# Kernel optimization log

Measured on AMD Instinct MI355X. Metric: run time of the kernel, lower is better.

## Reference

```python
import jax, jax.numpy as jnp
import numpy as np

IS, OS, H = 168, 24, 256           # input window, output horizon, state_hsize
TAU, MAXIMUM = 0.1, 1.0            # tau parameter (non-grad) and series maximum
DILS = [[1, 4], [16, 64]]          # ResidualDRNN groups of dilations


def _lstm(x, wih, whh, bih, bhh):
    """Single-layer LSTM over time-major x: (T, B, C). PyTorch gate order i,f,g,o."""
    def step(carry, xt):
        h, c = carry
        g = xt @ wih.T + h @ whh.T + (bih + bhh)
        i, f, gg, o = jnp.split(g, 4, axis=-1)
        c = jax.nn.sigmoid(f) * c + jax.nn.sigmoid(i) * jnp.tanh(gg)
        h = jax.nn.sigmoid(o) * jnp.tanh(c)
        return (h, c), h
    h0 = jnp.zeros((x.shape[1], H), x.dtype)
    _, hs = jax.lax.scan(step, (h0, h0), x)
    return hs


def _dilated_lstm(x, d, p):
    """Standard DRNN layer: pad T to multiple of d, interleave time into batch, run LSTM."""
    T, B, C = x.shape
    n = -(-T // d)
    xp = jnp.pad(x, ((0, n * d - T), (0, 0), (0, 0)))
    hd = _lstm(xp.reshape(n, d * B, C), *p)
    return hd.reshape(n * d, B, H)[:T]


def _forward(train, init_lev_sm, lstm_params, nl_w, nl_b, sc_w, sc_b):
    B, T = train.shape
    a = jax.nn.sigmoid(init_lev_sm[0])            # lev_sms (idxs are all 0 -> same scalar)
    floor = TAU * MAXIMUM                          # tau * maximum
    # --- exponential-smoothing level recurrence (sequential) ---
    lev0 = jnp.maximum(train[:, 0], floor)
    def step(lev, xt):
        new = jnp.maximum(a * xt + (1.0 - a) * lev, floor)
        return new, new
    _, rest = jax.lax.scan(step, lev0, train[:, 1:].T)
    levs = jnp.concatenate([lev0[None], rest], axis=0).T   # [B, T]
    # --- windowed normalization ---
    w_idx = jnp.arange(IS - 1, T)                           # W = T - IS + 1 window ends
    in_win = train[:, (w_idx - IS + 1)[:, None] + jnp.arange(IS)[None, :]]
    in_win = (in_win / levs[:, w_idx][:, :, None]).transpose(1, 0, 2)    # [W, B, IS]
    o_idx = jnp.arange(IS - 1, T - OS)                      # W_out = T - OS - IS + 1
    out_win = train[:, (o_idx + 1)[:, None] + jnp.arange(OS)[None, :]]
    out_win = (out_win / levs[:, o_idx][:, :, None]).transpose(1, 0, 2)  # [W_out, B, OS]
    # --- ResidualDRNN stack on window_input[:-OS] (time-major: windows are the sequence) ---
    x = in_win[:-OS]
    li = 0
    for g, dils in enumerate(DILS):
        residual = x
        h = x
        for d in dils:
            h = _dilated_lstm(h, d, lstm_params[li])
            li += 1
        x = h + residual if g > 0 else h                    # dropout p=0 -> identity
    x = jnp.tanh(x @ nl_w.T + nl_b)                         # add_nl_layer
    pred = x @ sc_w.T + sc_b                                # scoring
    return pred, out_win


def setup_inputs() -> dict:
    key = jax.random.key(0)
    ks = list(jax.random.split(key, 32))
    B, T = 32, 1024
    inp = {
        "train": jax.random.uniform(ks[0], (B, T), jnp.float32, 0.05, 1.0),
        "val": jax.random.uniform(ks[1], (B, T), jnp.float32, 0.05, 1.0),
        "test": jax.random.uniform(ks[2], (B, T), jnp.float32, 0.05, 1.0),
        "idxs": jnp.zeros((B,), jnp.int32),
        "init_lev_sm": jnp.array([0.5], jnp.float32),
    }
    sizes = [IS, H, H, H]  # input feature size of each of the 4 DRNN layers
    k = 3
    s = 1.0 / np.sqrt(H)
    for i, cin in enumerate(sizes):
        inp[f"wih{i}"] = jax.random.uniform(ks[k], (4 * H, cin), jnp.float32, -s, s); k += 1
        inp[f"whh{i}"] = jax.random.uniform(ks[k], (4 * H, H), jnp.float32, -s, s); k += 1
        inp[f"bih{i}"] = jax.random.uniform(ks[k], (4 * H,), jnp.float32, -s, s); k += 1
        inp[f"bhh{i}"] = jax.random.uniform(ks[k], (4 * H,), jnp.float32, -s, s); k += 1
    inp["nl_w"] = jax.random.uniform(ks[k], (H, H), jnp.float32, -s, s); k += 1
    inp["nl_b"] = jnp.zeros((H,), jnp.float32)
    inp["sc_w"] = jax.random.uniform(ks[k], (OS, H), jnp.float32, -s, s); k += 1
    inp["sc_b"] = jnp.zeros((OS,), jnp.float32)
    return inp


def reference(train, val, test, idxs, init_lev_sm,
              wih0, whh0, bih0, bhh0, wih1, whh1, bih1, bhh1,
              wih2, whh2, bih2, bhh2, wih3, whh3, bih3, bhh3,
              nl_w, nl_b, sc_w, sc_b):
    lstm_params = [(wih0, whh0, bih0, bhh0), (wih1, whh1, bih1, bhh1),
                   (wih2, whh2, bih2, bhh2), (wih3, whh3, bih3, bhh3)]
    # training path (validating=False, testing=False): only `train` is used
    return _forward(train, init_lev_sm, lstm_params, nl_w, nl_b, sc_w, sc_b)
```

## Files before the change

kernel.cpp:

```cpp
#include <hip/hip_runtime.h>
#include <hip/hip_fp16.h>
#include <math.h>

#define TT 833
#define GDIM 1024

typedef _Float16 f16x8 __attribute__((ext_vector_type(8)));
typedef float    f32x4 __attribute__((ext_vector_type(4)));

#if __has_builtin(__builtin_amdgcn_rcpf)
__device__ __forceinline__ float frcp(float x){ return __builtin_amdgcn_rcpf(x); }
#else
__device__ __forceinline__ float frcp(float x){ return 1.f/x; }
#endif

#if __has_builtin(__builtin_amdgcn_sdot4)
__device__ __forceinline__ int sdot4(unsigned a, unsigned b, int c){
  return __builtin_amdgcn_sdot4((int)a, (int)b, c, false);
}
#else
__device__ __forceinline__ int sdot4(unsigned a, unsigned b, int c){
  int ai = (int)a, bi = (int)b;
  c += ((ai<<24)>>24)*((bi<<24)>>24);
  c += ((ai<<16)>>24)*((bi<<16)>>24);
  c += ((ai<<8)>>24)*((bi<<8)>>24);
  c += (ai>>24)*(bi>>24);
  return c;
}
#endif


__global__ void levels_k(const float* __restrict__ train, const float* __restrict__ ism,
                         float* __restrict__ levs){
  int b = threadIdx.x;
  if (b >= 32) return;
  float a = 1.f/(1.f+expf(-ism[0]));
  const float* tr = train + b*1024;
  float* lv = levs + b*1024;
  float lev = fmaxf(tr[0], 0.1f);
  lv[0] = lev;
  for (int t = 1; t < 1024; ++t){
    lev = fmaxf(a*tr[t] + (1.f-a)*lev, 0.1f);
    lv[t] = lev;
  }
}

__global__ void win_x_k(const float* __restrict__ train, const float* __restrict__ levs,
                        float* __restrict__ x0){
  int idx = blockIdx.x*256 + threadIdx.x;
  int i = idx % 168;
  int r = idx / 168;
  int b = r & 31;
  int t = r >> 5;
  x0[idx] = train[b*1024 + t + i] / levs[b*1024 + t + 167];
}

__global__ void win_out_k(const float* __restrict__ train, const float* __restrict__ levs,
                          float* __restrict__ ow){
  int idx = blockIdx.x*256 + threadIdx.x;
  int o = idx % 24;
  int r = idx / 24;
  int b = r & 31;
  int t = r >> 5;
  ow[idx] = train[b*1024 + 168 + t + o] / levs[b*1024 + t + 167];
}

__global__ void permw_k(const float* __restrict__ wih, const float* __restrict__ bih,
                        const float* __restrict__ bhh, float* __restrict__ wP,
                        float* __restrict__ bP, int K){
  int t = blockIdx.x;
  int g = ((t & 3) << 8) + (t >> 2);
  for (int k = threadIdx.x; k < K; k += 256)
    wP[(size_t)t*K + k] = wih[(size_t)g*K + k];
  if (threadIdx.x == 0) bP[t] = bih[g] + bhh[g];
}

__global__ void packq_k(const float* __restrict__ w, uint4* __restrict__ wq,
                        float* __restrict__ sc){
  int t = blockIdx.x*256 + threadIdx.x;
  if (t >= 1024) return;
  int g = ((t & 3) << 8) + (t >> 2);
  const float* row = w + (size_t)g*256;
  float amax = 0.f;
  for (int k = 0; k < 256; ++k) amax = fmaxf(amax, fabsf(row[k]));
  amax = fmaxf(amax, 1e-20f);
  float s = amax/127.f, inv = 127.f/amax;
  sc[t] = s;
  for (int k16 = 0; k16 < 16; ++k16){
    union { uint4 u; signed char b[16]; } r;
    #pragma unroll
    for (int j = 0; j < 16; ++j){
      float q = rintf(row[k16*16 + j]*inv);
      q = fminf(fmaxf(q, -127.f), 127.f);
      r.b[j] = (signed char)q;
    }
    wq[(size_t)k16*1024 + t] = r.u;
  }
}

__global__ __launch_bounds__(256) void proj_mfma(
    const float* __restrict__ A, const float* __restrict__ W,
    const float* __restrict__ b1, const float* __restrict__ b2,
    float* __restrict__ C, int Mout, int K, int N, int dil, int act, int outHalf)
{
  __shared__ _Float16 As[128*40];
  __shared__ _Float16 Bs[128*40];
  const int tid = threadIdx.x;
  const int lane = tid & 63;
  const int w = tid >> 6, wr = w >> 1, wc = w & 1;
  const int m0 = blockIdx.y << 7, n0 = blockIdx.x << 7;

  const int rowA = tid >> 1;
  int srcrow;
  {
    int m = m0 + rowA;
    if (dil == 0) srcrow = (m < Mout) ? m : -1;
    else {
      int rows = dil << 5;
      int j = m / rows;
      int q = m - j*rows;
      int t = j*dil + (q >> 5);
      srcrow = (t < TT) ? ((t << 5) + (q & 31)) : -1;
    }
  }
  const int halfsel = tid & 1;
  const int nrow = n0 + rowA;

  f32x4 acc[4][4];
  #pragma unroll
  for (int i = 0; i < 4; ++i)
    #pragma unroll
    for (int j = 0; j < 4; ++j) acc[i][j] = (f32x4){0.f,0.f,0.f,0.f};

  const int nkt = (K + 31) >> 5;
  for (int kt = 0; kt < nkt; ++kt){
    const int k0 = (kt << 5) + halfsel*16;
    {
      union { uint4 u[2]; _Float16 h[16]; } tmp;
      if (srcrow >= 0 && k0 + 16 <= K){
        const float* s = A + (size_t)srcrow*K + k0;
        #pragma unroll
        for (int j = 0; j < 4; ++j){
          float4 v = *reinterpret_cast<const float4*>(s + j*4);
          tmp.h[j*4+0]=(_Float16)v.x; tmp.h[j*4+1]=(_Float16)v.y;
          tmp.h[j*4+2]=(_Float16)v.z; tmp.h[j*4+3]=(_Float16)v.w;
        }
      } else {
        const float* s = (srcrow >= 0) ? A + (size_t)srcrow*K : nullptr;
        #pragma unroll
        for (int j = 0; j < 16; ++j){
          int kk = k0 + j;
          tmp.h[j] = (s && kk < K) ? (_Float16)s[kk] : (_Float16)0.f;
        }
      }
      uint4* dst = reinterpret_cast<uint4*>(&As[rowA*40 + halfsel*16]);
      dst[0] = tmp.u[0]; dst[1] = tmp.u[1];
    }
    {
      union { uint4 u[2]; _Float16 h[16]; } tmp;
      if (k0 + 16 <= K){
        const float* s = W + (size_t)nrow*K + k0;
        #pragma unroll
        for (int j = 0; j < 4; ++j){
          float4 v = *reinterpret_cast<const float4*>(s + j*4);
          tmp.h[j*4+0]=(_Float16)v.x; tmp.h[j*4+1]=(_Float16)v.y;
          tmp.h[j*4+2]=(_Float16)v.z; tmp.h[j*4+3]=(_Float16)v.w;
        }
      } else {
        const float* s = W + (size_t)nrow*K;
        #pragma unroll
        for (int j = 0; j < 16; ++j){
          int kk = k0 + j;
          tmp.h[j] = (kk < K) ? (_Float16)s[kk] : (_Float16)0.f;
        }
      }
      uint4* dst = reinterpret_cast<uint4*>(&Bs[rowA*40 + halfsel*16]);
      dst[0] = tmp.u[0]; dst[1] = tmp.u[1];
    }
    __syncthreads();
    {
      const int kg = lane >> 4, r16 = lane & 15;
      f16x8 af[4], bf[4];
      #pragma unroll
      for (int mi = 0; mi < 4; ++mi)
        af[mi] = *reinterpret_cast<const f16x8*>(&As[(wr*64 + mi*16 + r16)*40 + kg*8]);
      #pragma unroll
      for (int nj = 0; nj < 4; ++nj)
        bf[nj] = *reinterpret_cast<const f16x8*>(&Bs[(wc*64 + nj*16 + r16)*40 + kg*8]);
      #pragma unroll
      for (int mi = 0; mi < 4; ++mi)
        #pragma unroll
        for (int nj = 0; nj < 4; ++nj)
          acc[mi][nj] = __builtin_amdgcn_mfma_f32_16x16x32_f16(af[mi], bf[nj], acc[mi][nj], 0, 0, 0);
    }
    __syncthreads();
  }
  #pragma unroll
  for (int mi = 0; mi < 4; ++mi){
    #pragma unroll
    for (int p = 0; p < 4; ++p){
      int mrow = m0 + wr*64 + mi*16 + (lane >> 4)*4 + p;
      if (mrow >= Mout) continue;
      #pragma unroll
      for (int nj = 0; nj < 4; ++nj){
        int ncol = n0 + wc*64 + nj*16 + (lane & 15);
        float v = acc[mi][nj][p] + b1[ncol] + (b2 ? b2[ncol] : 0.f);
        if (act) v = tanhf(v);
        if (outHalf) reinterpret_cast<__half*>(C)[(size_t)mrow*N + ncol] = __float2half(v);
        else C[(size_t)mrow*N + ncol] = v;
      }
    }
  }
}

template<int NR>
__global__ __launch_bounds__(512, 1) void srecr2_k(
    const uint4* __restrict__ wq, const float* __restrict__ scale,
    const __half* __restrict__ Gin,
    float* __restrict__ out, const float* __restrict__ res,
    int nsteps, int d, int rowsTotal)
{
  __shared__ __align__(16) unsigned int hq[2][NR][64];
  const int tid = threadIdx.x;
  const int s = tid & 1;
  const int j = tid >> 1;
  const int q0 = blockIdx.x*NR;
  const float sg0 = scale[2*tid]*(1.f/127.f);
  const float sg1 = scale[2*tid + 1]*(1.f/127.f);
  uint4 w0_[16], w1_[16];
  #pragma unroll
  for (int kk = 0; kk < 16; ++kk){
    w0_[kk] = wq[(size_t)kk*1024 + 2*tid];
    w1_[kk] = wq[(size_t)kk*1024 + 2*tid + 1];
  }
  float c[NR];
  #pragma unroll
  for (int rr = 0; rr < NR; ++rr) c[rr] = 0.f;
  for (int e = tid; e < 2*NR*64; e += 512) (&hq[0][0][0])[e] = 0u;
  __syncthreads();

  for (int step = 0; step < nsteps; ++step){
    const int cur = step & 1;
    const __half2* gbase = reinterpret_cast<const __half2*>(
        Gin + ((size_t)step*rowsTotal + q0)*GDIM);
    #pragma unroll
    for (int rr = 0; rr < NR; ++rr){
      __half2 g2 = gbase[rr*512 + tid];
      float gin0 = __half2float(__low2half(g2));
      float gin1 = __half2float(__high2half(g2));
      int a00 = 0, a01 = 0, a10 = 0, a11 = 0;
      #pragma unroll
      for (int k16 = 0; k16 < 8; ++k16){
        uint4 ha = *reinterpret_cast<const uint4*>(&hq[cur][rr][4*k16]);
        a00 = sdot4(w0_[k16].x, ha.x, a00); a00 = sdot4(w0_[k16].y, ha.y, a00);
        a00 = sdot4(w0_[k16].z, ha.z, a00); a00 = sdot4(w0_[k16].w, ha.w, a00);
        a10 = sdot4(w1_[k16].x, ha.x, a10); a10 = sdot4(w1_[k16].y, ha.y, a10);
        a10 = sdot4(w1_[k16].z, ha.z, a10); a10 = sdot4(w1_[k16].w, ha.w, a10);
        uint4 hb = *reinterpret_cast<const uint4*>(&hq[cur][rr][4*(k16 + 8)]);
        a01 = sdot4(w0_[k16+8].x, hb.x, a01); a01 = sdot4(w0_[k16+8].y, hb.y, a01);
        a01 = sdot4(w0_[k16+8].z, hb.z, a01); a01 = sdot4(w0_[k16+8].w, hb.w, a01);
        a11 = sdot4(w1_[k16+8].x, hb.x, a11); a11 = sdot4(w1_[k16+8].y, hb.y, a11);
        a11 = sdot4(w1_[k16+8].z, hb.z, a11); a11 = sdot4(w1_[k16+8].w, hb.w, a11);
      }
      float p0 = fmaf((float)(a00 + a01), sg0, gin0);
      float p1 = fmaf((float)(a10 + a11), sg1, gin1);
      float px0 = s ? p0 + p0 : p0;
      float t0 = frcp(1.f + __expf(-px0));
      float a0v = s ? fmaf(2.f, t0, -1.f) : t0;
      float a1v = frcp(1.f + __expf(-p1));
      float b0 = __shfl_xor(a0v, 1);
      float b1 = __shfl_xor(a1v, 1);
      float iv = s ? b0 : a0v;
      float fv = s ? b1 : a1v;
      float gv = s ? a0v : b0;
      float ov = s ? a1v : b1;
      float cn = fmaf(fv, c[rr], iv*gv);
      c[rr] = cn;
      if (s == 0){
        float e2 = __expf(-2.f*cn);
        float h = ov*(1.f - e2)*frcp(1.f + e2);
        int qh = (int)rintf(h*127.f);
        reinterpret_cast<signed char*>(&hq[cur^1][rr][0])[j] = (signed char)qh;
        int q = q0 + rr;
        int tg = step*d + (q >> 5);
        if (tg < TT){
          size_t oi = ((size_t)tg*32 + (q & 31))*256 + j;
          out[oi] = res ? (h + res[oi]) : h;
        }
      }
    }
    __syncthreads();
  }
}

template<int NR>
__global__ __launch_bounds__(1024) void srecq_k(
    const uint4* __restrict__ wq, const float* __restrict__ scale,
    const __half* __restrict__ Gin,
    float* __restrict__ out, const float* __restrict__ res,
    int nsteps, int d, int rowsTotal)
{
  __shared__ __align__(16) unsigned int hq[2][NR][64];
  const int tid = threadIdx.x;
  const int lane = tid & 63;
  const int base = lane & ~3;
  const int kg = tid & 3;
  const int j = tid >> 2;
  const int q0 = blockIdx.x*NR;
  const float sg = scale[tid]*(1.f/127.f);
  float c[NR];
  #pragma unroll
  for (int rr = 0; rr < NR; ++rr) c[rr] = 0.f;
  for (int e = tid; e < 2*NR*64; e += 1024) (&hq[0][0][0])[e] = 0u;
  __syncthreads();

  for (int step = 0; step < nsteps; ++step){
    const int cur = step & 1;
    float gin[NR];
    const __half* gbase = Gin + ((size_t)step*rowsTotal + q0)*GDIM;
    #pragma unroll
    for (int rr = 0; rr < NR; ++rr) gin[rr] = __half2float(gbase[rr*GDIM + tid]);
    int acc[NR];
    #pragma unroll
    for (int rr = 0; rr < NR; ++rr) acc[rr] = 0;
    #pragma unroll 4
    for (int k16 = 0; k16 < 16; ++k16){
      uint4 w = wq[(size_t)k16*1024 + tid];
      #pragma unroll
      for (int rr = 0; rr < NR; ++rr){
        uint4 h4 = *reinterpret_cast<const uint4*>(&hq[cur][rr][4*k16]);
        acc[rr] = sdot4(w.x, h4.x, acc[rr]);
        acc[rr] = sdot4(w.y, h4.y, acc[rr]);
        acc[rr] = sdot4(w.z, h4.z, acc[rr]);
        acc[rr] = sdot4(w.w, h4.w, acc[rr]);
      }
    }
    #pragma unroll
    for (int rr = 0; rr < NR; ++rr){
      float p = fmaf((float)acc[rr], sg, gin[rr]);
      float px = (kg == 2) ? p + p : p;
      float s = frcp(1.f + __expf(-px));
      float a = (kg == 2) ? fmaf(2.f, s, -1.f) : s;
      float iv = __shfl(a, base + 0);
      float fv = __shfl(a, base + 1);
      float gv = __shfl(a, base + 2);
      float ov = __shfl(a, base + 3);
      float cn = fmaf(fv, c[rr], iv*gv);
      c[rr] = cn;
      float e2 = __expf(-2.f*cn);
      float h = ov*(1.f - e2)*frcp(1.f + e2);
      if (kg == 0){
        int qh = (int)rintf(h*127.f);
        reinterpret_cast<signed char*>(&hq[cur^1][rr][0])[j] = (signed char)qh;
        int q = q0 + rr;
        int tg = step*d + (q >> 5);
        if (tg < TT){
          size_t oi = ((size_t)tg*32 + (q & 31))*256 + j;
          out[oi] = res ? (h + res[oi]) : h;
        }
      }
    }
    __syncthreads();
  }
}

__global__ __launch_bounds__(256) void sc_head(const float* __restrict__ xt, const float* __restrict__ w,
                        const float* __restrict__ bias, float* __restrict__ outp, int M){
  __shared__ float arow[8][256];
  int m0 = blockIdx.x << 3;
  int tid = threadIdx.x;
  #pragma unroll
  for (int i = 0; i < 8; ++i){
    int e = tid + (i << 8);
    int r = e >> 8, k = e & 255;
    arow[r][k] = (m0 + r < M) ? xt[(size_t)(m0 + r)*256 + k] : 0.f;
  }
  __syncthreads();
  int r = tid >> 5, n = tid & 31;
  if (n < 24 && (m0 + r) < M){
    float acc = bias[n];
    const float* wr = w + n*256;
    #pragma unroll 8
    for (int k = 0; k < 256; ++k) acc = fmaf(arow[r][k], wr[k], acc);
    outp[(size_t)(m0 + r)*24 + n] = acc;
  }
}

extern "C" void kernel_launch(void* const* d_in, const int* in_sizes, int n_in,
                              void* d_out, int out_size, void* d_ws, size_t ws_size,
                              hipStream_t stream){
  const float* train = (const float*)d_in[0];
  const float* ism   = (const float*)d_in[4];
  const float* wih[4] = {(const float*)d_in[5], (const float*)d_in[9], (const float*)d_in[13], (const float*)d_in[17]};
  const float* whh[4] = {(const float*)d_in[6], (const float*)d_in[10], (const float*)d_in[14], (const float*)d_in[18]};
  const float* bih[4] = {(const float*)d_in[7], (const float*)d_in[11], (const float*)d_in[15], (const float*)d_in[19]};
  const float* bhh[4] = {(const float*)d_in[8], (const float*)d_in[12], (const float*)d_in[16], (const float*)d_in[20]};
  const float* nl_w = (const float*)d_in[21];
  const float* nl_b = (const float*)d_in[22];
  const float* sc_w = (const float*)d_in[23];
  const float* sc_b = (const float*)d_in[24];
  float* out = (float*)d_out;

  float* ws = (float*)d_ws;
  size_t off = 0;
  float* levs = ws + off;   off += 32768;
  uint4* wqk[4];
  for (int l = 0; l < 4; ++l){ wqk[l] = (uint4*)(ws + off); off += 65536; }
  float* sck[4];
  for (int l = 0; l < 4; ++l){ sck[l] = ws + off; off += 1024; }
  float* wP[4];
  for (int l = 0; l < 4; ++l){ wP[l] = ws + off; off += 262144; }
  float* bP[4];
  for (int l = 0; l < 4; ++l){ bP[l] = ws + off; off += 1024; }
  float* x0 = ws + off;     off += (size_t)26656*168;
  __half* G  = (__half*)(ws + off); off += (size_t)28672*1024/2;
  float* h0 = ws + off;     off += (size_t)26656*256;
  float* h1 = ws + off;     off += (size_t)26656*256;
  float* h2 = ws + off;     off += (size_t)26656*256;
  (void)ws_size; (void)in_sizes; (void)n_in; (void)out_size;

  levels_k<<<1, 64, 0, stream>>>(train, ism, levs);
  win_x_k<<<17493, 256, 0, stream>>>(train, levs, x0);
  win_out_k<<<2499, 256, 0, stream>>>(train, levs, out + 639744);
  const int Kin[4] = {168, 256, 256, 256};
  for (int l = 0; l < 4; ++l){
    packq_k<<<4, 256, 0, stream>>>(whh[l], wqk[l], sck[l]);
    permw_k<<<1024, 256, 0, stream>>>(wih[l], bih[l], bhh[l], wP[l], bP[l], Kin[l]);
  }

  proj_mfma<<<dim3(8,209), 256, 0, stream>>>(x0, wP[0], bP[0], nullptr, (float*)G, 26656, 168, 1024, 0, 0, 1);
  srecr2_k<1><<<32, 512, 0, stream>>>(wqk[0], sck[0], G, h0, nullptr, 833, 1, 32);
  proj_mfma<<<dim3(8,209), 256, 0, stream>>>(h0, wP[1], bP[1], nullptr, (float*)G, 26752, 256, 1024, 4, 0, 1);
  srecr2_k<1><<<128, 512, 0, stream>>>(wqk[1], sck[1], G, h1, nullptr, 209, 4, 128);
  proj_mfma<<<dim3(8,212), 256, 0, stream>>>(h1, wP[2], bP[2], nullptr, (float*)G, 27136, 256, 1024, 16, 0, 1);
  srecr2_k<2><<<256, 512, 0, stream>>>(wqk[2], sck[2], G, h2, nullptr, 53, 16, 512);
  proj_mfma<<<dim3(8,224), 256, 0, stream>>>(h2, wP[3], bP[3], nullptr, (float*)G, 28672, 256, 1024, 64, 0, 1);
  srecq_k<8><<<256, 1024, 0, stream>>>(wqk[3], sck[3], G, h2, h1, 14, 64, 2048);
  proj_mfma<<<dim3(2,209), 256, 0, stream>>>(h2, nl_w, nl_b, nullptr, h0, 26656, 256, 256, 0, 1, 0);
  sc_head<<<3332, 256, 0, stream>>>(h0, sc_w, sc_b, out, 26656);
}
```

Measured before the change: 1.727 ms.

## Store intermediate activations and input weights in fp16 across the pipeline

Intermediate tensors (windowed input, LSTM hidden outputs, the nonlinear-layer output) and the input-projection weights are now stored as fp16 instead of fp32. The projection GEMM loads fp16 directly with 16-byte loads instead of converting from float. The residual path keeps an fp32 copy of layer 1's output for the final add. The levels recurrence is also vectorized with float4 loads and stores. This halves memory traffic for the projections and recurrence outputs, at the cost of slightly lower precision in stored activations and the tanh output.

```diff
diff --git a/kernel.cpp b/kernel.cpp
--- a/kernel.cpp
+++ b/kernel.cpp
@@ -35,24 +35,29 @@
   int b = threadIdx.x;
   if (b >= 32) return;
   float a = 1.f/(1.f+expf(-ism[0]));
-  const float* tr = train + b*1024;
-  float* lv = levs + b*1024;
-  float lev = fmaxf(tr[0], 0.1f);
-  lv[0] = lev;
-  for (int t = 1; t < 1024; ++t){
-    lev = fmaxf(a*tr[t] + (1.f-a)*lev, 0.1f);
-    lv[t] = lev;
+  const float4* tr4 = reinterpret_cast<const float4*>(train + b*1024);
+  float4* lv4 = reinterpret_cast<float4*>(levs + b*1024);
+  float lev = 0.f;
+  for (int i = 0; i < 256; ++i){
+    float4 v = tr4[i];
+    float4 o;
+    if (i == 0) o.x = lev = fmaxf(v.x, 0.1f);
+    else        o.x = lev = fmaxf(fmaf(a, v.x, (1.f-a)*lev), 0.1f);
+    o.y = lev = fmaxf(fmaf(a, v.y, (1.f-a)*lev), 0.1f);
+    o.z = lev = fmaxf(fmaf(a, v.z, (1.f-a)*lev), 0.1f);
+    o.w = lev = fmaxf(fmaf(a, v.w, (1.f-a)*lev), 0.1f);
+    lv4[i] = o;
   }
 }
 
 __global__ void win_x_k(const float* __restrict__ train, const float* __restrict__ levs,
-                        float* __restrict__ x0){
+                        __half* __restrict__ x0){
   int idx = blockIdx.x*256 + threadIdx.x;
   int i = idx % 168;
   int r = idx / 168;
   int b = r & 31;
   int t = r >> 5;
-  x0[idx] = train[b*1024 + t + i] / levs[b*1024 + t + 167];
+  x0[idx] = __float2half(train[b*1024 + t + i] / levs[b*1024 + t + 167]);
 }
 
 __global__ void win_out_k(const float* __restrict__ train, const float* __restrict__ levs,
@@ -66,13 +71,18 @@
 }
 
 __global__ void permw_k(const float* __restrict__ wih, const float* __restrict__ bih,
-                        const float* __restrict__ bhh, float* __restrict__ wP,
+                        const float* __restrict__ bhh, __half* __restrict__ wP,
                         float* __restrict__ bP, int K){
   int t = blockIdx.x;
   int g = ((t & 3) << 8) + (t >> 2);
   for (int k = threadIdx.x; k < K; k += 256)
-    wP[(size_t)t*K + k] = wih[(size_t)g*K + k];
+    wP[(size_t)t*K + k] = __float2half(wih[(size_t)g*K + k]);
   if (threadIdx.x == 0) bP[t] = bih[g] + bhh[g];
+}
+
+__global__ void cvth_k(const float* __restrict__ s, __half* __restrict__ d, int n){
+  int i = blockIdx.x*256 + threadIdx.x;
+  if (i < n) d[i] = __float2half(s[i]);
 }
 
 __global__ void packq_k(const float* __restrict__ w, uint4* __restrict__ wq,
@@ -99,9 +109,9 @@
 }
 
 __global__ __launch_bounds__(256) void proj_mfma(
-    const float* __restrict__ A, const float* __restrict__ W,
-    const float* __restrict__ b1, const float* __restrict__ b2,
-    float* __restrict__ C, int Mout, int K, int N, int dil, int act, int outHalf)
+    const _Float16* __restrict__ A, const _Float16* __restrict__ W,
+    const float* __restrict__ b1,
+    void* __restrict__ C, int Mout, int K, int N, int dil, int act, int outHalf)
 {
   __shared__ _Float16 As[128*40];
   __shared__ _Float16 Bs[128*40];
@@ -138,19 +148,14 @@
     {
       union { uint4 u[2]; _Float16 h[16]; } tmp;
       if (srcrow >= 0 && k0 + 16 <= K){
-        const float* s = A + (size_t)srcrow*K + k0;
-        #pragma unroll
-        for (int j = 0; j < 4; ++j){
-          float4 v = *reinterpret_cast<const float4*>(s + j*4);
-          tmp.h[j*4+0]=(_Float16)v.x; tmp.h[j*4+1]=(_Float16)v.y;
-          tmp.h[j*4+2]=(_Float16)v.z; tmp.h[j*4+3]=(_Float16)v.w;
-        }
+        const uint4* s = reinterpret_cast<const uint4*>(A + (size_t)srcrow*K + k0);
+        tmp.u[0] = s[0]; tmp.u[1] = s[1];
       } else {
-        const float* s = (srcrow >= 0) ? A + (size_t)srcrow*K : nullptr;
+        const _Float16* s = (srcrow >= 0) ? A + (size_t)srcrow*K : nullptr;
         #pragma unroll
         for (int j = 0; j < 16; ++j){
           int kk = k0 + j;
-          tmp.h[j] = (s && kk < K) ? (_Float16)s[kk] : (_Float16)0.f;
+          tmp.h[j] = (s && kk < K) ? s[kk] : (_Float16)0.f;
         }
       }
       uint4* dst = reinterpret_cast<uint4*>(&As[rowA*40 + halfsel*16]);
@@ -159,19 +164,14 @@
     {
       union { uint4 u[2]; _Float16 h[16]; } tmp;
       if (k0 + 16 <= K){
-        const float* s = W + (size_t)nrow*K + k0;
-        #pragma unroll
-        for (int j = 0; j < 4; ++j){
-          float4 v = *reinterpret_cast<const float4*>(s + j*4);
-          tmp.h[j*4+0]=(_Float16)v.x; tmp.h[j*4+1]=(_Float16)v.y;
-          tmp.h[j*4+2]=(_Float16)v.z; tmp.h[j*4+3]=(_Float16)v.w;
-        }
+        const uint4* s = reinterpret_cast<const uint4*>(W + (size_t)nrow*K + k0);
+        tmp.u[0] = s[0]; tmp.u[1] = s[1];
       } else {
-        const float* s = W + (size_t)nrow*K;
+        const _Float16* s = W + (size_t)nrow*K;
         #pragma unroll
         for (int j = 0; j < 16; ++j){
           int kk = k0 + j;
-          tmp.h[j] = (kk < K) ? (_Float16)s[kk] : (_Float16)0.f;
+          tmp.h[j] = (kk < K) ? s[kk] : (_Float16)0.f;
         }
       }
       uint4* dst = reinterpret_cast<uint4*>(&Bs[rowA*40 + halfsel*16]);
@@ -204,10 +204,10 @@
       #pragma unroll
       for (int nj = 0; nj < 4; ++nj){
         int ncol = n0 + wc*64 + nj*16 + (lane & 15);
-        float v = acc[mi][nj][p] + b1[ncol] + (b2 ? b2[ncol] : 0.f);
+        float v = acc[mi][nj][p] + b1[ncol];
         if (act) v = tanhf(v);
         if (outHalf) reinterpret_cast<__half*>(C)[(size_t)mrow*N + ncol] = __float2half(v);
-        else C[(size_t)mrow*N + ncol] = v;
+        else reinterpret_cast<float*>(C)[(size_t)mrow*N + ncol] = v;
       }
     }
   }
@@ -217,7 +217,7 @@
 __global__ __launch_bounds__(512, 1) void srecr2_k(
     const uint4* __restrict__ wq, const float* __restrict__ scale,
     const __half* __restrict__ Gin,
-    float* __restrict__ out, const float* __restrict__ res,
+    __half* __restrict__ outh, float* __restrict__ outf,
     int nsteps, int d, int rowsTotal)
 {
   __shared__ __align__(16) unsigned int hq[2][NR][64];
@@ -285,7 +285,8 @@
         int tg = step*d + (q >> 5);
         if (tg < TT){
           size_t oi = ((size_t)tg*32 + (q & 31))*256 + j;
-          out[oi] = res ? (h + res[oi]) : h;
+          outh[oi] = __float2half(h);
+          if (outf) outf[oi] = h;
         }
       }
     }
@@ -297,7 +298,7 @@
 __global__ __launch_bounds__(1024) void srecq_k(
     const uint4* __restrict__ wq, const float* __restrict__ scale,
     const __half* __restrict__ Gin,
-    float* __restrict__ out, const float* __restrict__ res,
+    __half* __restrict__ outh, const float* __restrict__ res,
     int nsteps, int d, int rowsTotal)
 {
   __shared__ __align__(16) unsigned int hq[2][NR][64];
@@ -339,8 +340,8 @@
     for (int rr = 0; rr < NR; ++rr){
       float p = fmaf((float)acc[rr], sg, gin[rr]);
       float px = (kg == 2) ? p + p : p;
-      float s = frcp(1.f + __expf(-px));
-      float a = (kg == 2) ? fmaf(2.f, s, -1.f) : s;
+      float sv = frcp(1.f + __expf(-px));
+      float a = (kg == 2) ? fmaf(2.f, sv, -1.f) : sv;
       float iv = __shfl(a, base + 0);
       float fv = __shfl(a, base + 1);
       float gv = __shfl(a, base + 2);
@@ -356,7 +357,7 @@
         int tg = step*d + (q >> 5);
         if (tg < TT){
           size_t oi = ((size_t)tg*32 + (q & 31))*256 + j;
-          out[oi] = res ? (h + res[oi]) : h;
+          outh[oi] = __float2half(h + res[oi]);
         }
       }
     }
@@ -364,7 +365,7 @@
   }
 }
 
-__global__ __launch_bounds__(256) void sc_head(const float* __restrict__ xt, const float* __restrict__ w,
+__global__ __launch_bounds__(256) void sc_head(const __half* __restrict__ xt, const float* __restrict__ w,
                         const float* __restrict__ bias, float* __restrict__ outp, int M){
   __shared__ float arow[8][256];
   int m0 = blockIdx.x << 3;
@@ -373,7 +374,7 @@
   for (int i = 0; i < 8; ++i){
     int e = tid + (i << 8);
     int r = e >> 8, k = e & 255;
-    arow[r][k] = (m0 + r < M) ? xt[(size_t)(m0 + r)*256 + k] : 0.f;
+    arow[r][k] = (m0 + r < M) ? __half2float(xt[(size_t)(m0 + r)*256 + k]) : 0.f;
   }
   __syncthreads();
   int r = tid >> 5, n = tid & 31;
@@ -408,34 +409,39 @@
   for (int l = 0; l < 4; ++l){ wqk[l] = (uint4*)(ws + off); off += 65536; }
   float* sck[4];
   for (int l = 0; l < 4; ++l){ sck[l] = ws + off; off += 1024; }
-  float* wP[4];
-  for (int l = 0; l < 4; ++l){ wP[l] = ws + off; off += 262144; }
+  __half* wPh[4];
+  for (int l = 0; l < 4; ++l){ wPh[l] = (__half*)(ws + off); off += 131072; }
   float* bP[4];
   for (int l = 0; l < 4; ++l){ bP[l] = ws + off; off += 1024; }
-  float* x0 = ws + off;     off += (size_t)26656*168;
-  __half* G  = (__half*)(ws + off); off += (size_t)28672*1024/2;
-  float* h0 = ws + off;     off += (size_t)26656*256;
-  float* h1 = ws + off;     off += (size_t)26656*256;
-  float* h2 = ws + off;     off += (size_t)26656*256;
+  __half* nlwh = (__half*)(ws + off); off += 32768;
+  __half* x0h = (__half*)(ws + off);  off += (size_t)26656*168/2;
+  __half* G   = (__half*)(ws + off);  off += (size_t)28672*1024/2;
+  __half* h0h = (__half*)(ws + off);  off += (size_t)26656*256/2;
+  __half* h1h = (__half*)(ws + off);  off += (size_t)26656*256/2;
+  float*  h1f = ws + off;             off += (size_t)26656*256;
+  __half* h2h = (__half*)(ws + off);  off += (size_t)26656*256/2;
+  __half* xfh = (__half*)(ws + off);  off += (size_t)26656*256/2;
+  __half* xth = (__half*)(ws + off);  off += (size_t)26656*256/2;
   (void)ws_size; (void)in_sizes; (void)n_in; (void)out_size;
 
   levels_k<<<1, 64, 0, stream>>>(train, ism, levs);
-  win_x_k<<<17493, 256, 0, stream>>>(train, levs, x0);
+  win_x_k<<<17493, 256, 0, stream>>>(train, levs, x0h);
   win_out_k<<<2499, 256, 0, stream>>>(train, levs, out + 639744);
   const int Kin[4] = {168, 256, 256, 256};
   for (int l = 0; l < 4; ++l){
     packq_k<<<4, 256, 0, stream>>>(whh[l], wqk[l], sck[l]);
-    permw_k<<<1024, 256, 0, stream>>>(wih[l], bih[l], bhh[l], wP[l], bP[l], Kin[l]);
-  }
-
-  proj_mfma<<<dim3(8,209), 256, 0, stream>>>(x0, wP[0], bP[0], nullptr, (float*)G, 26656, 168, 1024, 0, 0, 1);
-  srecr2_k<1><<<32, 512, 0, stream>>>(wqk[0], sck[0], G, h0, nullptr, 833, 1, 32);
-  proj_mfma<<<dim3(8,209), 256, 0, stream>>>(h0, wP[1], bP[1], nullptr, (float*)G, 26752, 256, 1024, 4, 0, 1);
-  srecr2_k<1><<<128, 512, 0, stream>>>(wqk[1], sck[1], G, h1, nullptr, 209, 4, 128);
-  proj_mfma<<<dim3(8,212), 256, 0, stream>>>(h1, wP[2], bP[2], nullptr, (float*)G, 27136, 256, 1024, 16, 0, 1);
-  srecr2_k<2><<<256, 512, 0, stream>>>(wqk[2], sck[2], G, h2, nullptr, 53, 16, 512);
-  proj_mfma<<<dim3(8,224), 256, 0, stream>>>(h2, wP[3], bP[3], nullptr, (float*)G, 28672, 256, 1024, 64, 0, 1);
-  srecq_k<8><<<256, 1024, 0, stream>>>(wqk[3], sck[3], G, h2, h1, 14, 64, 2048);
-  proj_mfma<<<dim3(2,209), 256, 0, stream>>>(h2, nl_w, nl_b, nullptr, h0, 26656, 256, 256, 0, 1, 0);
-  sc_head<<<3332, 256, 0, stream>>>(h0, sc_w, sc_b, out, 26656);
-}
+    permw_k<<<1024, 256, 0, stream>>>(wih[l], bih[l], bhh[l], wPh[l], bP[l], Kin[l]);
+  }
+  cvth_k<<<256, 256, 0, stream>>>(nl_w, nlwh, 65536);
+
+  proj_mfma<<<dim3(8,209), 256, 0, stream>>>((const _Float16*)x0h, (const _Float16*)wPh[0], bP[0], G, 26656, 168, 1024, 0, 0, 1);
+  srecr2_k<1><<<32, 512, 0, stream>>>(wqk[0], sck[0], G, h0h, nullptr, 833, 1, 32);
+  proj_mfma<<<dim3(8,209), 256, 0, stream>>>((const _Float16*)h0h, (const _Float16*)wPh[1], bP[1], G, 26752, 256, 1024, 4, 0, 1);
+  srecr2_k<1><<<128, 512, 0, stream>>>(wqk[1], sck[1], G, h1h, h1f, 209, 4, 128);
+  proj_mfma<<<dim3(8,212), 256, 0, stream>>>((const _Float16*)h1h, (const _Float16*)wPh[2], bP[2], G, 27136, 256, 1024, 16, 0, 1);
+  srecr2_k<2><<<256, 512, 0, stream>>>(wqk[2], sck[2], G, h2h, nullptr, 53, 16, 512);
+  proj_mfma<<<dim3(8,224), 256, 0, stream>>>((const _Float16*)h2h, (const _Float16*)wPh[3], bP[3], G, 28672, 256, 1024, 64, 0, 1);
+  srecq_k<8><<<256, 1024, 0, stream>>>(wqk[3], sck[3], G, xfh, h1f, 14, 64, 2048);
+  proj_mfma<<<dim3(2,209), 256, 0, stream>>>((const _Float16*)xfh, (const _Float16*)nlwh, nl_b, xth, 26656, 256, 256, 0, 1, 1);
+  sc_head<<<3332, 256, 0, stream>>>(xth, sc_w, sc_b, out, 26656);
+}
```

Result: faster. 1.662 ms (-3.7%).
